# Optimization experiments

Measured on AMD Instinct MI355X. Metric: run time of the kernel, lower is better.

The kernel has to match this reference:

```python
import math
import jax, jax.numpy as jnp
import numpy as np

NH, NKV, HD, THETA = 32, 8, 128, 500000.0

def rotate_half(x):
    x1, x2 = jnp.split(x, 2, axis=-1)
    return jnp.concatenate((-x2, x1), axis=-1)

def rope_cos_sin(seq_len, dim, base, dtype):
    inv_freq = 1.0 / (base ** (jnp.arange(0, dim, 2, dtype=jnp.float32) / dim))
    t = jnp.arange(seq_len, dtype=jnp.float32)
    freqs = jnp.outer(t, inv_freq)              # [S, dim/2]
    emb = jnp.concatenate((freqs, freqs), -1)   # [S, dim]
    return jnp.cos(emb).astype(dtype), jnp.sin(emb).astype(dtype)

def setup_inputs() -> dict:
    key = jax.random.key(0)
    ks = jax.random.split(key, 5)
    B, S, H = 1, 2048, 4096
    sc = 1.0 / math.sqrt(H)
    return {
        'x':  jax.random.normal(ks[0], (B, S, H), jnp.float32),
        'wq': jax.random.normal(ks[1], (H, H), jnp.float32) * sc,
        'wk': jax.random.normal(ks[2], (NKV * HD, H), jnp.float32) * sc,
        'wv': jax.random.normal(ks[3], (NKV * HD, H), jnp.float32) * sc,
        'wo': jax.random.normal(ks[4], (H, H), jnp.float32) * sc,
    }

def attention(x, wq, wk, wv, wo):
    B, S, H = x.shape
    n_rep = NH // NKV
    q = (x @ wq.T).reshape(B, S, NH, HD).transpose(0, 2, 1, 3)    # [B,NH,S,HD]
    k = (x @ wk.T).reshape(B, S, NKV, HD).transpose(0, 2, 1, 3)   # [B,NKV,S,HD]
    v = (x @ wv.T).reshape(B, S, NKV, HD).transpose(0, 2, 1, 3)
    cos, sin = rope_cos_sin(S, HD, THETA, x.dtype)                # [S,HD]
    cos = cos[None, None]; sin = sin[None, None]
    q = q * cos + rotate_half(q) * sin
    k = k * cos + rotate_half(k) * sin
    k = jnp.repeat(k, n_rep, axis=1)                               # [B,NH,S,HD]
    v = jnp.repeat(v, n_rep, axis=1)
    scores = jnp.einsum('bhqd,bhkd->bhqk', q, k) / math.sqrt(HD)
    causal = jnp.tril(jnp.ones((S, S), dtype=bool))
    scores = jnp.where(causal, scores, jnp.finfo(scores.dtype).min)
    probs = jax.nn.softmax(scores, axis=-1)
    out = jnp.einsum('bhqk,bhkd->bhqd', probs, v)                  # [B,NH,S,HD]
    out = out.transpose(0, 2, 1, 3).reshape(B, S, H)
    return out @ wo.T

def reference(x, wq, wk, wv, wo):
    return attention(x, wq, wk, wv, wo)
```

## Files before the change

### kernel.cpp

```cpp
#include <hip/hip_runtime.h>
#include <hip/hip_bf16.h>
#include <math.h>

typedef __bf16 bf16x8 __attribute__((ext_vector_type(8)));
typedef __bf16 bf16x4 __attribute__((ext_vector_type(4)));
typedef unsigned short u16x8 __attribute__((ext_vector_type(8)));
typedef float  f32x4  __attribute__((ext_vector_type(4)));

constexpr int kS   = 2048;
constexpr int kH   = 4096;
constexpr int kNH  = 32;
constexpr int kNKV = 8;
constexpr int kHD  = 128;
constexpr int kQKV = kH + 2 * kNKV * kHD;
constexpr int kKOff = kH;
constexpr int kVOff = kH + kNKV * kHD;

__global__ void cast_bf16(const float* __restrict__ in, __bf16* __restrict__ out, int n4) {
    int i = blockIdx.x * blockDim.x + threadIdx.x;
    if (i < n4) {
        float4 f = ((const float4*)in)[i];
        bf16x4 o;
        o[0] = (__bf16)f.x; o[1] = (__bf16)f.y; o[2] = (__bf16)f.z; o[3] = (__bf16)f.w;
        ((bf16x4*)out)[i] = o;
    }
}

__global__ void cast_all(const float* __restrict__ x, const float* __restrict__ wq,
                         const float* __restrict__ wk, const float* __restrict__ wv,
                         __bf16* __restrict__ xb, __bf16* __restrict__ wqkv) {
    int i = blockIdx.x * 256 + threadIdx.x;
    float4 f;
    __bf16* dst;
    int di;
    if (i < (1 << 21)) {
        f = ((const float4*)x)[i];
        dst = xb; di = i;
    } else {
        int j = i - (1 << 21);
        const float4* s = (j < (1 << 22)) ? ((const float4*)wq + j)
                        : (j < (5 << 20)) ? ((const float4*)wk + (j - (1 << 22)))
                                          : ((const float4*)wv + (j - (5 << 20)));
        f = *s;
        dst = wqkv; di = j;
    }
    bf16x4 o;
    o[0] = (__bf16)f.x; o[1] = (__bf16)f.y; o[2] = (__bf16)f.z; o[3] = (__bf16)f.w;
    ((bf16x4*)dst)[di] = o;
}

__device__ inline void gld16(const __bf16* g, __bf16* l) {
    __builtin_amdgcn_global_load_lds((const __attribute__((address_space(1))) void*)g,
                                     (__attribute__((address_space(3))) void*)l, 16, 0, 0);
}

constexpr int GBK = 32, GBN = 256;

template <typename OutT, int GBM>
__global__ __launch_bounds__(512, 2) void gemm8(const __bf16* __restrict__ A,
                                                const __bf16* __restrict__ B,
                                                OutT* __restrict__ C,
                                                int M, int N, int K, int nbx) {
    static_assert(GBM == 256 || GBM == 128, "");
    constexpr int PH  = GBM / 128;
    constexpr int FM  = GBM / 32;
    constexpr int AG  = GBM / 128;
    constexpr int BG  = 2;
    constexpr int GPK = AG + BG;
    constexpr int ASZ = GBM * GBK;
    constexpr int BSZ = GBN * GBK;

    __shared__ __align__(16) __bf16 Ab[3][ASZ];
    __shared__ __align__(16) __bf16 Bb[3][BSZ];

    const int tid = threadIdx.x, w = tid >> 6, lane = tid & 63;
    const int lr = lane & 15, g = lane >> 4;

    const int nwg = (int)gridDim.x;
    const int bid = (int)blockIdx.x;
    const int id2 = (bid & 7) * (nwg >> 3) + (bid >> 3);
    const int m0 = (id2 / nbx) * GBM, n0 = (id2 % nbx) * GBN;

    const int wm = (w >> 2) * (GBM / 2), wn = (w & 3) * 64;

    const __bf16* ga[AG]; int la[AG];
    const __bf16* gb[BG]; int lb[BG];
#pragma unroll
    for (int a = 0; a < AG; a++) {
        int G = a * 512 + tid, row = G >> 2;
        int lg = (G & 3) ^ ((row >> 1) & 3);
        ga[a] = A + (size_t)(m0 + row) * K + lg * 8;
        la[a] = G * 8;
    }
#pragma unroll
    for (int b = 0; b < BG; b++) {
        int G = b * 512 + tid, row = G >> 2;
        int lg = (G & 3) ^ ((row >> 1) & 3);
        gb[b] = B + (size_t)(n0 + row) * K + lg * 8;
        lb[b] = G * 8;
    }

    int pao[FM], pbo[4];
    const int sw = (lr >> 1) & 3;
#pragma unroll
    for (int i = 0; i < FM; i++) pao[i] = (wm + i * 16 + lr) * GBK + ((g ^ sw) * 8);
#pragma unroll
    for (int j = 0; j < 4; j++)  pbo[j] = (wn + j * 16 + lr) * GBK + ((g ^ sw) * 8);

    f32x4 acc[FM][4];
#pragma unroll
    for (int i = 0; i < FM; i++)
#pragma unroll
        for (int j = 0; j < 4; j++) acc[i][j] = (f32x4)(0.f);

    const int NT = K / GBK;

#pragma unroll
    for (int z = 0; z < 2; z++) {
#pragma unroll
        for (int a = 0; a < AG; a++) gld16(ga[a] + z * GBK, &Ab[z][la[a]]);
#pragma unroll
        for (int b = 0; b < BG; b++) gld16(gb[b] + z * GBK, &Bb[z][lb[b]]);
    }
    if constexpr (GPK == 4) asm volatile("s_waitcnt vmcnt(4)" ::: "memory");
    else                    asm volatile("s_waitcnt vmcnt(3)" ::: "memory");
    __builtin_amdgcn_s_barrier();

    int q = 0;
    for (int Z = 0; Z < NT; ++Z) {
        const int qs = (q + 2 >= 3) ? q - 1 : q + 2;
        const bool stg = Z < NT - 2;
#pragma unroll
        for (int p = 0; p < PH; p++) {
            bf16x8 af[4], bfr[4];
#pragma unroll
            for (int i = 0; i < 4; i++) af[i]  = *(const bf16x8*)&Ab[q][pao[p * 4 + i]];
#pragma unroll
            for (int j = 0; j < 4; j++) bfr[j] = *(const bf16x8*)&Bb[q][pbo[j]];

            if (stg) {
                if constexpr (PH == 2) {
                    if (p == 0) {
#pragma unroll
                        for (int a = 0; a < AG; a++) gld16(ga[a] + (Z + 2) * GBK, &Ab[qs][la[a]]);
                    } else {
#pragma unroll
                        for (int b = 0; b < BG; b++) gld16(gb[b] + (Z + 2) * GBK, &Bb[qs][lb[b]]);
                    }
                } else {
#pragma unroll
                    for (int a = 0; a < AG; a++) gld16(ga[a] + (Z + 2) * GBK, &Ab[qs][la[a]]);
#pragma unroll
                    for (int b = 0; b < BG; b++) gld16(gb[b] + (Z + 2) * GBK, &Bb[qs][lb[b]]);
                }
            }

            __builtin_amdgcn_s_barrier();
            __builtin_amdgcn_s_setprio(1);
#pragma unroll
            for (int i = 0; i < 4; i++)
#pragma unroll
                for (int j = 0; j < 4; j++)
                    acc[p * 4 + i][j] = __builtin_amdgcn_mfma_f32_16x16x32_bf16(
                        af[i], bfr[j], acc[p * 4 + i][j], 0, 0, 0);
            __builtin_amdgcn_s_setprio(0);

            if (p == PH - 1) {
                if (Z < NT - 2) {
                    if constexpr (GPK == 4) asm volatile("s_waitcnt vmcnt(4)" ::: "memory");
                    else                    asm volatile("s_waitcnt vmcnt(3)" ::: "memory");
                } else if (Z == NT - 2) {
                    asm volatile("s_waitcnt vmcnt(0)" ::: "memory");
                }
            }
            __builtin_amdgcn_s_barrier();
        }
        q = (q + 1 == 3) ? 0 : q + 1;
    }

    const int cr = g * 4, cc = lr;
#pragma unroll
    for (int i = 0; i < FM; i++)
#pragma unroll
        for (int j = 0; j < 4; j++) {
            OutT* Cp = C + (size_t)(m0 + wm + i * 16 + cr) * N + (n0 + wn + j * 16 + cc);
#pragma unroll
            for (int r = 0; r < 4; r++) Cp[(size_t)r * N] = (OutT)acc[i][j][r];
        }
}

__global__ void rope_qkv(__bf16* __restrict__ qkv) {
    int idx  = blockIdx.x * 256 + threadIdx.x;
    int d8   = idx & 7;
    int rest = idx >> 3;
    int hh   = rest % (kNH + kNKV);
    int s    = rest / (kNH + kNKV);
    __bf16* base = qkv + (size_t)s * kQKV + ((hh < kNH) ? hh * kHD : kKOff + (hh - kNH) * kHD);
    float sc = (hh < kNH) ? 0.088388347648318447f : 1.0f;
    bf16x8 va = *(const bf16x8*)(base + d8 * 8);
    bf16x8 vb = *(const bf16x8*)(base + 64 + d8 * 8);
    bf16x8 ra, rb;
#pragma unroll
    for (int j = 0; j < 8; j++) {
        int d = d8 * 8 + j;
        float rev = (float)s * exp2f(fmaf((float)d, -0.2958057589f, -2.6514961295f));
        rev -= floorf(rev);
        float ang = rev * 6.28318530718f;
        float sn = __sinf(ang), cs = __cosf(ang);
        float a = (float)va[j], b = (float)vb[j];
        ra[j] = (__bf16)((a * cs - b * sn) * sc);
        rb[j] = (__bf16)((b * cs + a * sn) * sc);
    }
    *(bf16x8*)(base + d8 * 8)      = ra;
    *(bf16x8*)(base + 64 + d8 * 8) = rb;
}

constexpr int VTP = 72;

__global__ __launch_bounds__(256) void flash_attn(const __bf16* __restrict__ qkv,
                                                  __bf16* __restrict__ ob) {
    __shared__ __align__(16) __bf16 Ks[64 * 128];
    __shared__ __align__(16) __bf16 Vt[128 * VTP];
    __shared__ __align__(16) __bf16 Ps[4 * 16 * 64];

    const int tid  = threadIdx.x;
    const int wave = tid >> 6, lane = tid & 63;
    const int bx   = blockIdx.x;
    const int kvh  = bx & 7;
    const int qt   = 127 - (bx >> 3);
    const int h    = kvh * 4 + wave;
    const int r    = lane & 15, g = lane >> 4;
    const int r7   = r & 7;
    const int qglob = qt * 16 + r;

    __bf16* Pw = Ps + wave * 16 * 64;
    const __bf16* kbase = qkv + kKOff + kvh * kHD;
    const __bf16* vbase = qkv + kVOff + kvh * kHD;

    int krow[4], kgc[4];
#pragma unroll
    for (int c = 0; c < 4; c++) {
        krow[c] = wave * 16 + c * 4 + (lane >> 4);
        kgc[c]  = (lane & 15) ^ (krow[c] & 15);
    }

    bf16x8 qfrag[4];
    const __bf16* qrow = qkv + (size_t)(qt * 16 + r) * kQKV + h * kHD + g * 8;
#pragma unroll
    for (int c = 0; c < 4; c++) qfrag[c] = *(const bf16x8*)(qrow + c * 32);

    f32x4 o[8];
#pragma unroll
    for (int dt = 0; dt < 8; dt++) o[dt] = (f32x4)(0.f);
    float mrow = -3.0e38f, lrow = 0.f;

    const int nkt = qt / 4 + 1;
    for (int kt = 0; kt < nkt; ++kt) {
#pragma unroll
        for (int c = 0; c < 4; c++)
            gld16(kbase + (size_t)(kt * 64 + krow[c]) * kQKV + kgc[c] * 8,
                  Ks + (wave * 4 + c) * 512);
#pragma unroll
        for (int i = 0; i < 2; i++) {
            int task = i * 256 + tid;
            int p = task & 31, c = task >> 5;
            const __bf16* v0 = vbase + (size_t)(kt * 64 + 2 * p) * kQKV + c * 8;
            u16x8 a = __builtin_bit_cast(u16x8, *(const bf16x8*)v0);
            u16x8 b = __builtin_bit_cast(u16x8, *(const bf16x8*)(v0 + kQKV));
#pragma unroll
            for (int j = 0; j < 8; j++) {
                unsigned int pk = (unsigned int)a[j] | ((unsigned int)b[j] << 16);
                *(unsigned int*)(Vt + (c * 8 + j) * VTP + 2 * p) = pk;
            }
        }
        __syncthreads();

        f32x4 st[4];
#pragma unroll
        for (int t = 0; t < 4; t++) st[t] = (f32x4)(0.f);
#pragma unroll
        for (int c = 0; c < 4; c++) {
#pragma unroll
            for (int t = 0; t < 4; t++) {
                bf16x8 kf = *(const bf16x8*)&Ks[(t * 16 + r) * 128 + (((c * 4 + g) ^ r) * 8)];
                st[t] = __builtin_amdgcn_mfma_f32_16x16x32_bf16(kf, qfrag[c], st[t], 0, 0, 0);
            }
        }

        if (kt == nkt - 1) {
#pragma unroll
            for (int t = 0; t < 4; t++)
#pragma unroll
                for (int reg = 0; reg < 4; reg++) {
                    int key = kt * 64 + t * 16 + g * 4 + reg;
                    if (key > qglob) st[t][reg] = -3.0e38f;
                }
        }

        float mloc = -3.0e38f;
#pragma unroll
        for (int t = 0; t < 4; t++)
#pragma unroll
            for (int reg = 0; reg < 4; reg++) mloc = fmaxf(mloc, st[t][reg]);
        mloc = fmaxf(mloc, __shfl_xor(mloc, 16));
        mloc = fmaxf(mloc, __shfl_xor(mloc, 32));
        float mnew  = fmaxf(mrow, mloc);
        float alpha = __expf(mrow - mnew);
        mrow = mnew;
        float lsum = 0.f;
#pragma unroll
        for (int t = 0; t < 4; t++)
#pragma unroll
            for (int reg = 0; reg < 4; reg++) {
                float pv = __expf(st[t][reg] - mnew);
                st[t][reg] = pv;
                lsum += pv;
            }
        lsum += __shfl_xor(lsum, 16);
        lsum += __shfl_xor(lsum, 32);
        lrow = lrow * alpha + lsum;

        float ar[4];
#pragma unroll
        for (int reg = 0; reg < 4; reg++) ar[reg] = __shfl(alpha, g * 4 + reg);
#pragma unroll
        for (int dt = 0; dt < 8; dt++)
#pragma unroll
            for (int reg = 0; reg < 4; reg++) o[dt][reg] *= ar[reg];

#pragma unroll
        for (int t = 0; t < 4; t++) {
            bf16x4 pb;
#pragma unroll
            for (int j = 0; j < 4; j++) pb[j] = (__bf16)st[t][j];
            int p8 = t * 4 + g;
            *(bf16x4*)&Pw[r * 64 + (((p8 >> 1) ^ r7) * 8) + ((p8 & 1) * 4)] = pb;
        }
        __asm__ volatile("s_waitcnt lgkmcnt(0)" ::: "memory");

#pragma unroll
        for (int kc = 0; kc < 2; kc++) {
            bf16x8 pf = *(const bf16x8*)&Pw[r * 64 + (((kc * 4 + g) ^ r7) * 8)];
#pragma unroll
            for (int dt = 0; dt < 8; dt++) {
                bf16x8 vf = *(const bf16x8*)&Vt[(dt * 16 + r) * VTP + kc * 32 + g * 8];
                o[dt] = __builtin_amdgcn_mfma_f32_16x16x32_bf16(pf, vf, o[dt], 0, 0, 0);
            }
        }
        __syncthreads();
    }

    float linv = 1.f / lrow;
    float lr4[4];
#pragma unroll
    for (int reg = 0; reg < 4; reg++) lr4[reg] = __shfl(linv, g * 4 + reg);
#pragma unroll
    for (int dt = 0; dt < 8; dt++)
#pragma unroll
        for (int reg = 0; reg < 4; reg++) {
            int qq = g * 4 + reg, dd = dt * 16 + r;
            ob[(size_t)(qt * 16 + qq) * kH + h * kHD + dd] = (__bf16)(o[dt][reg] * lr4[reg]);
        }
}

extern "C" void kernel_launch(void* const* d_in, const int* in_sizes, int n_in,
                              void* d_out, int out_size, void* d_ws, size_t ws_size,
                              hipStream_t stream) {
    const float* x  = (const float*)d_in[0];
    const float* wq = (const float*)d_in[1];
    const float* wk = (const float*)d_in[2];
    const float* wv = (const float*)d_in[3];
    const float* wo = (const float*)d_in[4];
    float* out = (float*)d_out;

    char* p = (char*)d_ws;
    auto alloc = [&](size_t bytes) {
        char* r = p;
        p += (bytes + 255) & ~(size_t)255;
        return r;
    };
    __bf16* xb    = (__bf16*)alloc((size_t)kS * kH * 2);
    __bf16* wqkvb = (__bf16*)alloc((size_t)kQKV * kH * 2);
    __bf16* qkv   = (__bf16*)alloc((size_t)kS * kQKV * 2);
    __bf16* ao    = xb;
    __bf16* wob   = wqkvb;

    cast_all<<<dim3(1 << 15), 256, 0, stream>>>(x, wq, wk, wv, xb, wqkvb);

    gemm8<__bf16, 256><<<dim3((kQKV / GBN) * (kS / 256)), 512, 0, stream>>>(
        xb, wqkvb, qkv, kS, kQKV, kH, kQKV / GBN);

    rope_qkv<<<dim3(kS * (kNH + kNKV) * 8 / 256), 256, 0, stream>>>(qkv);

    cast_bf16<<<dim3((kH * kH / 4) / 256), 256, 0, stream>>>(wo, wob, kH * kH / 4);

    flash_attn<<<dim3(kNKV * (kS / 16)), 256, 0, stream>>>(qkv, ao);

    gemm8<float, 128><<<dim3((kH / GBN) * (kS / 128)), 512, 0, stream>>>(
        ao, wob, out, kS, kH, kH, kH / GBN);
}
```

Baseline: 496.3 us.

## Retile GEMMs to 128-row tiles with wider N and a 4-stage LDS pipeline

The GEMM kernel now fixes the M tile at 128 rows and makes the N tile a template parameter: 384 for the QKV projection and 256 for the output projection. Each wave holds a 64xN/4 register block. The two-phase inner loop is replaced by a single phase per K step. The LDS ring grows from three to four buffers, so loads are issued three tiles ahead with matching vmcnt waits. For the QKV GEMM this gives 256 workgroups instead of 192, a better fit to the CU count, and deeper prefetch hides global latency. The cost is much more LDS per block (about 128KB for QKV), which likely leaves one block per CU, plus more accumulator registers.

```diff
diff --git a/kernel.cpp b/kernel.cpp
--- a/kernel.cpp
+++ b/kernel.cpp
@@ -54,24 +54,23 @@
                                      (__attribute__((address_space(3))) void*)l, 16, 0, 0);
 }
 
-constexpr int GBK = 32, GBN = 256;
-
-template <typename OutT, int GBM>
+constexpr int GBK = 32, GBM = 128;
+
+template <typename OutT, int GBN>
 __global__ __launch_bounds__(512, 2) void gemm8(const __bf16* __restrict__ A,
                                                 const __bf16* __restrict__ B,
                                                 OutT* __restrict__ C,
                                                 int M, int N, int K, int nbx) {
-    static_assert(GBM == 256 || GBM == 128, "");
-    constexpr int PH  = GBM / 128;
-    constexpr int FM  = GBM / 32;
-    constexpr int AG  = GBM / 128;
-    constexpr int BG  = 2;
-    constexpr int GPK = AG + BG;
+    constexpr int FM  = 4;
+    constexpr int FN  = GBN / 64;
+    constexpr int AL  = GBM / 128;
+    constexpr int BL  = GBN / 128;
+    constexpr int GPK = AL + BL;
     constexpr int ASZ = GBM * GBK;
     constexpr int BSZ = GBN * GBK;
 
-    __shared__ __align__(16) __bf16 Ab[3][ASZ];
-    __shared__ __align__(16) __bf16 Bb[3][BSZ];
+    __shared__ __align__(16) __bf16 Ab[4][ASZ];
+    __shared__ __align__(16) __bf16 Bb[4][BSZ];
 
     const int tid = threadIdx.x, w = tid >> 6, lane = tid & 63;
     const int lr = lane & 15, g = lane >> 4;
@@ -81,108 +80,94 @@
     const int id2 = (bid & 7) * (nwg >> 3) + (bid >> 3);
     const int m0 = (id2 / nbx) * GBM, n0 = (id2 % nbx) * GBN;
 
-    const int wm = (w >> 2) * (GBM / 2), wn = (w & 3) * 64;
-
-    const __bf16* ga[AG]; int la[AG];
-    const __bf16* gb[BG]; int lb[BG];
-#pragma unroll
-    for (int a = 0; a < AG; a++) {
+    const int wm = (w >> 2) * 64, wn = (w & 3) * (GBN / 4);
+
+    const __bf16* ga[AL]; int la[AL];
+    const __bf16* gb[BL]; int lb[BL];
+#pragma unroll
+    for (int a = 0; a < AL; a++) {
         int G = a * 512 + tid, row = G >> 2;
         int lg = (G & 3) ^ ((row >> 1) & 3);
         ga[a] = A + (size_t)(m0 + row) * K + lg * 8;
         la[a] = G * 8;
     }
 #pragma unroll
-    for (int b = 0; b < BG; b++) {
+    for (int b = 0; b < BL; b++) {
         int G = b * 512 + tid, row = G >> 2;
         int lg = (G & 3) ^ ((row >> 1) & 3);
         gb[b] = B + (size_t)(n0 + row) * K + lg * 8;
         lb[b] = G * 8;
     }
 
-    int pao[FM], pbo[4];
+    int pao[FM], pbo[FN];
     const int sw = (lr >> 1) & 3;
 #pragma unroll
     for (int i = 0; i < FM; i++) pao[i] = (wm + i * 16 + lr) * GBK + ((g ^ sw) * 8);
 #pragma unroll
-    for (int j = 0; j < 4; j++)  pbo[j] = (wn + j * 16 + lr) * GBK + ((g ^ sw) * 8);
-
-    f32x4 acc[FM][4];
+    for (int j = 0; j < FN; j++) pbo[j] = (wn + j * 16 + lr) * GBK + ((g ^ sw) * 8);
+
+    f32x4 acc[FM][FN];
 #pragma unroll
     for (int i = 0; i < FM; i++)
 #pragma unroll
-        for (int j = 0; j < 4; j++) acc[i][j] = (f32x4)(0.f);
+        for (int j = 0; j < FN; j++) acc[i][j] = (f32x4)(0.f);
 
     const int NT = K / GBK;
 
 #pragma unroll
-    for (int z = 0; z < 2; z++) {
-#pragma unroll
-        for (int a = 0; a < AG; a++) gld16(ga[a] + z * GBK, &Ab[z][la[a]]);
-#pragma unroll
-        for (int b = 0; b < BG; b++) gld16(gb[b] + z * GBK, &Bb[z][lb[b]]);
-    }
-    if constexpr (GPK == 4) asm volatile("s_waitcnt vmcnt(4)" ::: "memory");
-    else                    asm volatile("s_waitcnt vmcnt(3)" ::: "memory");
+    for (int z = 0; z < 3; z++) {
+#pragma unroll
+        for (int a = 0; a < AL; a++) gld16(ga[a] + z * GBK, &Ab[z][la[a]]);
+#pragma unroll
+        for (int b = 0; b < BL; b++) gld16(gb[b] + z * GBK, &Bb[z][lb[b]]);
+    }
+    if constexpr (GPK == 4) asm volatile("s_waitcnt vmcnt(8)" ::: "memory");
+    else                    asm volatile("s_waitcnt vmcnt(6)" ::: "memory");
     __builtin_amdgcn_s_barrier();
 
-    int q = 0;
     for (int Z = 0; Z < NT; ++Z) {
-        const int qs = (q + 2 >= 3) ? q - 1 : q + 2;
-        const bool stg = Z < NT - 2;
-#pragma unroll
-        for (int p = 0; p < PH; p++) {
-            bf16x8 af[4], bfr[4];
-#pragma unroll
-            for (int i = 0; i < 4; i++) af[i]  = *(const bf16x8*)&Ab[q][pao[p * 4 + i]];
-#pragma unroll
-            for (int j = 0; j < 4; j++) bfr[j] = *(const bf16x8*)&Bb[q][pbo[j]];
-
-            if (stg) {
-                if constexpr (PH == 2) {
-                    if (p == 0) {
-#pragma unroll
-                        for (int a = 0; a < AG; a++) gld16(ga[a] + (Z + 2) * GBK, &Ab[qs][la[a]]);
-                    } else {
-#pragma unroll
-                        for (int b = 0; b < BG; b++) gld16(gb[b] + (Z + 2) * GBK, &Bb[qs][lb[b]]);
-                    }
-                } else {
-#pragma unroll
-                    for (int a = 0; a < AG; a++) gld16(ga[a] + (Z + 2) * GBK, &Ab[qs][la[a]]);
-#pragma unroll
-                    for (int b = 0; b < BG; b++) gld16(gb[b] + (Z + 2) * GBK, &Bb[qs][lb[b]]);
-                }
-            }
-
-            __builtin_amdgcn_s_barrier();
-            __builtin_amdgcn_s_setprio(1);
-#pragma unroll
-            for (int i = 0; i < 4; i++)
-#pragma unroll
-                for (int j = 0; j < 4; j++)
-                    acc[p * 4 + i][j] = __builtin_amdgcn_mfma_f32_16x16x32_bf16(
-                        af[i], bfr[j], acc[p * 4 + i][j], 0, 0, 0);
-            __builtin_amdgcn_s_setprio(0);
-
-            if (p == PH - 1) {
-                if (Z < NT - 2) {
-                    if constexpr (GPK == 4) asm volatile("s_waitcnt vmcnt(4)" ::: "memory");
-                    else                    asm volatile("s_waitcnt vmcnt(3)" ::: "memory");
-                } else if (Z == NT - 2) {
-                    asm volatile("s_waitcnt vmcnt(0)" ::: "memory");
-                }
-            }
-            __builtin_amdgcn_s_barrier();
-        }
-        q = (q + 1 == 3) ? 0 : q + 1;
+        const int q = Z & 3, qs = (Z + 3) & 3;
+
+        bf16x8 af[FM], bfr[FN];
+#pragma unroll
+        for (int i = 0; i < FM; i++) af[i]  = *(const bf16x8*)&Ab[q][pao[i]];
+#pragma unroll
+        for (int j = 0; j < FN; j++) bfr[j] = *(const bf16x8*)&Bb[q][pbo[j]];
+
+        if (Z < NT - 3) {
+#pragma unroll
+            for (int a = 0; a < AL; a++) gld16(ga[a] + (Z + 3) * GBK, &Ab[qs][la[a]]);
+#pragma unroll
+            for (int b = 0; b < BL; b++) gld16(gb[b] + (Z + 3) * GBK, &Bb[qs][lb[b]]);
+        }
+
+        __builtin_amdgcn_s_barrier();
+        __builtin_amdgcn_s_setprio(1);
+#pragma unroll
+        for (int i = 0; i < FM; i++)
+#pragma unroll
+            for (int j = 0; j < FN; j++)
+                acc[i][j] = __builtin_amdgcn_mfma_f32_16x16x32_bf16(
+                    af[i], bfr[j], acc[i][j], 0, 0, 0);
+        __builtin_amdgcn_s_setprio(0);
+
+        if (Z < NT - 3) {
+            if constexpr (GPK == 4) asm volatile("s_waitcnt vmcnt(8)" ::: "memory");
+            else                    asm volatile("s_waitcnt vmcnt(6)" ::: "memory");
+        } else if (Z == NT - 3) {
+            if constexpr (GPK == 4) asm volatile("s_waitcnt vmcnt(4)" ::: "memory");
+            else                    asm volatile("s_waitcnt vmcnt(3)" ::: "memory");
+        } else if (Z == NT - 2) {
+            asm volatile("s_waitcnt vmcnt(0)" ::: "memory");
+        }
+        __builtin_amdgcn_s_barrier();
     }
 
     const int cr = g * 4, cc = lr;
 #pragma unroll
     for (int i = 0; i < FM; i++)
 #pragma unroll
-        for (int j = 0; j < 4; j++) {
+        for (int j = 0; j < FN; j++) {
             OutT* Cp = C + (size_t)(m0 + wm + i * 16 + cr) * N + (n0 + wn + j * 16 + cc);
 #pragma unroll
             for (int r = 0; r < 4; r++) Cp[(size_t)r * N] = (OutT)acc[i][j][r];
@@ -387,8 +372,8 @@
 
     cast_all<<<dim3(1 << 15), 256, 0, stream>>>(x, wq, wk, wv, xb, wqkvb);
 
-    gemm8<__bf16, 256><<<dim3((kQKV / GBN) * (kS / 256)), 512, 0, stream>>>(
-        xb, wqkvb, qkv, kS, kQKV, kH, kQKV / GBN);
+    gemm8<__bf16, 384><<<dim3((kS / GBM) * (kQKV / 384)), 512, 0, stream>>>(
+        xb, wqkvb, qkv, kS, kQKV, kH, kQKV / 384);
 
     rope_qkv<<<dim3(kS * (kNH + kNKV) * 8 / 256), 256, 0, stream>>>(qkv);
 
@@ -396,6 +381,6 @@
 
     flash_attn<<<dim3(kNKV * (kS / 16)), 256, 0, stream>>>(qkv, ao);
 
-    gemm8<float, 128><<<dim3((kH / GBN) * (kS / 128)), 512, 0, stream>>>(
-        ao, wob, out, kS, kH, kH, kH / GBN);
-}
+    gemm8<float, 256><<<dim3((kS / GBM) * (kH / 256)), 512, 0, stream>>>(
+        ao, wob, out, kS, kH, kH, kH / 256);
+}
```

Result: faster. 474.9 us (-4.3%).
